# Performance work log

Hardware: AMD Instinct MI355X
Metric: run time of the kernel (lower is better)

Reference implementation:

```python
import jax, jax.numpy as jnp
import numpy as np
import math

H = 65
W = 65
NH = 8
DIM_K = 512
DIM_Q = 512
DIM_HID = NH * DIM_K  # 4096; forced by V.view(bsz,-1,num_heads,dim_K)
RW = W // 2 + 1  # 33, rfft2 last-dim size


def _conv2d(x, w, pad):
    # x: NCHW, w: OIHW
    return jax.lax.conv_general_dilated(
        x, w, window_strides=(1, 1), padding=[(pad, pad), (pad, pad)],
        dimension_numbers=('NCHW', 'OIHW', 'NCHW'))


def _filter_branch(x, w1, w2, w3, Wd, bd):
    # x: (1, DIM_K, H, W)
    f = _conv2d(x, w1, 0)                                  # 1x1 conv
    f = _conv2d(jax.nn.relu(f), w2, 1) + f                 # 3x3 conv + residual
    f = jax.nn.relu(_conv2d(jax.nn.relu(f), w3, 0))        # 1x1 -> (1, NH, H, W)
    f = f.reshape(NH, H * W) @ Wd.T + bd                   # down-proj to (NH, 65*33)
    return f.reshape(NH, H, RW)


def setup_inputs() -> dict:
    key = jax.random.key(0)
    ks = jax.random.split(key, 20)
    s = 0.02
    f32 = jnp.float32
    inp = {
        'Q': jax.random.normal(ks[0], (1, 1, DIM_Q), f32),
        'K': jax.random.normal(ks[1], (1, DIM_K, H, W), f32),
        'Wq': jax.random.normal(ks[2], (DIM_HID, DIM_Q), f32) * s,
        'bq': jnp.zeros((DIM_HID,), f32),
        'Wk': jax.random.normal(ks[3], (DIM_HID, DIM_K), f32) * s,
        'bk': jnp.zeros((DIM_HID,), f32),
        'Wv': jax.random.normal(ks[4], (DIM_HID, DIM_K), f32) * s,
        'bv': jnp.zeros((DIM_HID,), f32),
        'Wo': jax.random.normal(ks[5], (DIM_K, DIM_HID), f32) * s,
        'bo': jnp.zeros((DIM_K,), f32),
        'amp1': jax.random.normal(ks[6], (DIM_K, DIM_K, 1, 1), f32) * 0.05,
        'amp2': jax.random.normal(ks[7], (DIM_K, DIM_K, 3, 3), f32) * 0.02,
        'amp3': jax.random.normal(ks[8], (NH, DIM_K, 1, 1), f32) * 0.05,
        'pha1': jax.random.normal(ks[9], (DIM_K, DIM_K, 1, 1), f32) * 0.05,
        'pha2': jax.random.normal(ks[10], (DIM_K, DIM_K, 3, 3), f32) * 0.02,
        'pha3': jax.random.normal(ks[11], (NH, DIM_K, 1, 1), f32) * 0.05,
        'Wd1': jax.random.normal(ks[12], (H * RW, H * W), f32) * s,
        'bd1': jnp.zeros((H * RW,), f32),
        'Wd2': jax.random.normal(ks[13], (H * RW, H * W), f32) * s,
        'bd2': jnp.zeros((H * RW,), f32),
    }
    return inp


def reference(Q, K, Wq, bq, Wk, bk, Wv, bv, Wo, bo,
              amp1, amp2, amp3, pha1, pha2, pha3, Wd1, bd1, Wd2, bd2):
    bsz, h, w = K.shape[0], K.shape[2], K.shape[3]
    dk = DIM_HID // NH
    qrt = K
    Kp = jnp.transpose(K, (0, 2, 3, 1))                      # (1, h, w, DIM_K)
    q = Q @ Wq.T + bq                                        # (1, 1, DIM_HID)
    k = Kp @ Wk.T + bk                                       # (1, h, w, DIM_HID)
    v = Kp @ Wv.T + bv
    q = q.reshape(bsz, -1, NH, dk).transpose(0, 2, 1, 3)     # (1, NH, 1, dk)
    k = k.reshape(bsz, -1, NH, dk).transpose(0, 2, 1, 3)     # (1, NH, h*w, dk)
    v = v.reshape(bsz, -1, NH, DIM_K).transpose(0, 2, 1, 3)  # (1, NH, h*w, DIM_K)
    A = jnp.einsum('bhqd,bhkd->bhqk', q, k) / math.sqrt(DIM_K)
    amp_F = _filter_branch(qrt, amp1, amp2, amp3, Wd1, bd1)  # (NH, h, w//2+1)
    pha_F = _filter_branch(qrt, pha1, pha2, pha3, Wd2, bd2)
    A = A.reshape(NH, h, w)
    Af = jnp.fft.rfft2(A, axes=(-2, -1))                     # backward norm (default)
    amp = amp_F * jnp.abs(Af)
    pha = pha_F * jnp.angle(Af)
    Af = jax.lax.complex(amp * jnp.cos(pha), amp * jnp.sin(pha))
    A = jnp.fft.irfft2(Af, s=(h, w), axes=(-2, -1))
    A = jax.nn.softmax(A.reshape(bsz, NH, 1, -1), axis=-1)   # (1, NH, 1, h*w)
    x = jnp.einsum('bhqk,bhkd->bhqd', A, v)                  # (1, NH, 1, DIM_K)
    x = x.reshape(1, NH * DIM_K)
    return x @ Wo.T + bo                                     # (1, DIM_K)
```

## Files before the change

kernel.cpp:

```cpp
#include <hip/hip_runtime.h>
#include <hip/hip_bf16.h>

#define NP 4225
#define PR 2145

typedef __attribute__((ext_vector_type(8))) short short8;
typedef __attribute__((ext_vector_type(4))) float f32x4;
typedef __attribute__((ext_vector_type(4))) unsigned int u32x4;

__device__ inline float bf2f(unsigned short u) {
    union { unsigned int i; float f; } x; x.i = ((unsigned int)u) << 16; return x.f;
}
__device__ inline unsigned short f2bf(float f) {
    union { float f; unsigned int i; } x; x.f = f;
    unsigned int r = x.i + 0x7fff + ((x.i >> 16) & 1);
    return (unsigned short)(r >> 16);
}
__device__ inline u32x4 relu8(u32x4 v) {
    #pragma unroll
    for (int i = 0; i < 4; i++) {
        unsigned int s = v[i] & 0x80008000u;
        v[i] &= ~((s >> 15) * 0xFFFFu);
    }
    return v;
}


__global__ __launch_bounds__(256) void k_q(const float* __restrict__ Q,
                                           const float* __restrict__ Wq,
                                           const float* __restrict__ bq,
                                           float* __restrict__ qv)
{
    int wid = threadIdx.x >> 6, lane = threadIdx.x & 63;
    int j = blockIdx.x * 4 + wid;
    float s = 0.f;
    for (int i = lane; i < 512; i += 64) s += Q[i] * Wq[j * 512 + i];
    #pragma unroll
    for (int off = 32; off; off >>= 1) s += __shfl_down(s, off);
    if (lane == 0) qv[j] = s + bq[j];
}

__global__ __launch_bounds__(256) void k_qk3(const float* __restrict__ qv,
                                             const float* __restrict__ Wk,
                                             float* __restrict__ qkp)
{
    int c = blockIdx.x * 256 + threadIdx.x;
    int h = blockIdx.y, dz = blockIdx.z;
    __shared__ float qs[32];
    if (threadIdx.x < 32) qs[threadIdx.x] = qv[h * 512 + dz * 32 + threadIdx.x];
    __syncthreads();
    float s = 0.f;
    #pragma unroll 8
    for (int d = 0; d < 32; d++)
        s += qs[d] * Wk[(size_t)(h * 512 + dz * 32 + d) * 512 + c];
    qkp[(dz * 8 + h) * 512 + c] = s;
}

__global__ __launch_bounds__(512) void k_qb(const float* __restrict__ q,
                                            const float* __restrict__ bk,
                                            float* __restrict__ qb)
{
    int h = threadIdx.x >> 6, lane = threadIdx.x & 63;
    float s = 0.f;
    for (int d = lane; d < 512; d += 64) s += q[h * 512 + d] * bk[h * 512 + d];
    #pragma unroll
    for (int off = 32; off; off >>= 1) s += __shfl_down(s, off);
    if (lane == 0) qb[h] = s;
}

__global__ __launch_bounds__(256) void k_alogits3(const float* __restrict__ qkp,
                                                  const float* __restrict__ K,
                                                  float* __restrict__ Ap)
{
    __shared__ float sqk[8][16];
    int tid = threadIdx.x;
    int cz = blockIdx.y;
    if (tid < 128) {
        int hh = tid >> 4, cc = tid & 15;
        float s = 0.f;
        #pragma unroll
        for (int dz = 0; dz < 16; dz++) s += qkp[(dz * 8 + hh) * 512 + cz * 16 + cc];
        sqk[hh][cc] = s;
    }
    __syncthreads();
    int p = blockIdx.x * 256 + tid;
    bool ok = p < NP;
    float acc[8] = {};
    #pragma unroll
    for (int cc = 0; cc < 16; cc++) {
        float kv = ok ? K[(size_t)(cz * 16 + cc) * NP + p] : 0.f;
        #pragma unroll
        for (int h = 0; h < 8; h++) acc[h] += sqk[h][cc] * kv;
    }
    if (ok) {
        #pragma unroll
        for (int h = 0; h < 8; h++) Ap[(size_t)(cz * 8 + h) * NP + p] = acc[h];
    }
}

__global__ __launch_bounds__(256) void k_areduce(const float* __restrict__ Ap,
                                                 const float* __restrict__ qb,
                                                 float* __restrict__ A)
{
    int p = blockIdx.x * 256 + threadIdx.x;
    int h = blockIdx.y;
    if (p >= NP) return;
    float s = 0.f;
    #pragma unroll 8
    for (int cz = 0; cz < 32; cz++) s += Ap[(size_t)(cz * 8 + h) * NP + p];
    const float sc = 0.04419417382415922f;
    A[h * NP + p] = (s + qb[h]) * sc;
}


__global__ __launch_bounds__(256) void k_cast2(const float* __restrict__ a,
                                               const float* __restrict__ b,
                                               unsigned short* __restrict__ o)
{
    int i = blockIdx.x * 256 + threadIdx.x;
    int br = blockIdx.y;
    const float* src = br ? b : a;
    o[(size_t)br * 262144 + i] = f2bf(src[i]);
}

__global__ __launch_bounds__(256) void k_packW2(const float* __restrict__ a,
                                                const float* __restrict__ b,
                                                unsigned short* __restrict__ o)
{
    int i = blockIdx.x * 256 + threadIdx.x;
    int br = blockIdx.y;
    int m = i >> 9, c = i & 511;
    const float* src = (br ? b : a) + (size_t)i * 9;
    unsigned short* dst = o + (size_t)br * 512 * 4608;
    #pragma unroll
    for (int t = 0; t < 9; t++) dst[(size_t)m * 4608 + t * 512 + c] = f2bf(src[t]);
}


__global__ __launch_bounds__(256) void k_conv1T(const float* __restrict__ K,
                                                const unsigned short* __restrict__ w1b2,
                                                unsigned short* __restrict__ f0b2)
{
    __shared__ unsigned short As[2][64 * 64];
    __shared__ unsigned short Bs[2][128 * 64];
    int tid = threadIdx.x;
    int bid = blockIdx.x;
    int u = bid & 7;
    int t = bid >> 3;
    int bmi = u * 9 + t % 9;
    if (bmi >= 67) return;
    int combo = t / 9;
    int bm = bmi * 64;
    int bn = (combo & 3) * 128;
    int br = combo >> 2;
    const unsigned short* w1 = w1b2 + (size_t)br * 262144;
    unsigned short* f0 = f0b2 + (size_t)br * NP * 512;
    int lane = tid & 63;
    int w = tid >> 6;
    int wp = (w >> 1) * 32, wm = (w & 1) * 64;
    int rb = tid >> 1, hb = tid & 1;
    int ct = tid >> 4, p4 = (tid & 15) * 4;

    f32x4 acc[2][4];
    #pragma unroll
    for (int i = 0; i < 2; i++)
        #pragma unroll
        for (int j = 0; j < 4; j++) acc[i][j] = (f32x4){0.f, 0.f, 0.f, 0.f};

    float aA[16], aB[16];
    u32x4 bA[4], bB[4];

    auto loadRegs = [&](int kc, float (&ar)[16], u32x4 (&brg)[4]) {
        int c0 = kc * 64;
        #pragma unroll
        for (int pass = 0; pass < 4; pass++) {
            int cl = pass * 16 + ct;
            const float* src = K + (size_t)(c0 + cl) * NP + bm + p4;
            #pragma unroll
            for (int j = 0; j < 4; j++)
                ar[pass * 4 + j] = (bm + p4 + j < NP) ? src[j] : 0.f;
        }
        const unsigned short* brow = w1 + (size_t)(bn + rb) * 512 + c0 + hb * 32;
        #pragma unroll
        for (int j = 0; j < 4; j++) brg[j] = *(const u32x4*)(brow + j * 8);
    };
    auto writeS = [&](int buf, float (&ar)[16], u32x4 (&brg)[4]) {
        #pragma unroll
        for (int pass = 0; pass < 4; pass++) {
            int cl = pass * 16 + ct;
            #pragma unroll
            for (int j = 0; j < 4; j++) {
                int row = p4 + j;
                int byte = (row * 128 + cl * 2) ^ ((row & 7) << 4);
                *(unsigned short*)((char*)As[buf] + byte) = f2bf(ar[pass * 4 + j]);
            }
        }
        int bb = rb * 128 + hb * 64;
        #pragma unroll
        for (int j = 0; j < 4; j++)
            *(u32x4*)((char*)Bs[buf] + ((bb + j * 16) ^ ((rb & 7) << 4))) = brg[j];
    };
    auto mfmaStep = [&](int buf) {
        __builtin_amdgcn_s_setprio(1);
        #pragma unroll
        for (int ks = 0; ks < 2; ks++) {
            short8 af[2], bfr[4];
            #pragma unroll
            for (int fi = 0; fi < 2; fi++) {
                int row = wp + fi * 16 + (lane & 15);
                int byte = row * 128 + ((ks * 64 + ((lane >> 4) * 16)) ^ ((row & 7) << 4));
                af[fi] = *(const short8*)((char*)As[buf] + byte);
            }
            #pragma unroll
            for (int fj = 0; fj < 4; fj++) {
                int n = wm + fj * 16 + (lane & 15);
                int byte = n * 128 + ((ks * 64 + ((lane >> 4) * 16)) ^ ((n & 7) << 4));
                bfr[fj] = *(const short8*)((char*)Bs[buf] + byte);
            }
            #pragma unroll
            for (int fi = 0; fi < 2; fi++)
                #pragma unroll
                for (int fj = 0; fj < 4; fj++)
                    acc[fi][fj] = __builtin_amdgcn_mfma_f32_16x16x32_bf16(af[fi], bfr[fj], acc[fi][fj], 0, 0, 0);
        }
        __builtin_amdgcn_s_setprio(0);
    };

    loadRegs(0, aA, bA);
    loadRegs(1, aB, bB);
    writeS(0, aA, bA);
    __syncthreads();
    for (int ib = 0; ib < 4; ib++) {
        int it = 2 * ib;
        if (it + 2 < 8) loadRegs(it + 2, aA, bA);
        mfmaStep(0);
        writeS(1, aB, bB);
        __syncthreads();
        if (it + 3 < 8) loadRegs(it + 3, aB, bB);
        mfmaStep(1);
        if (it + 2 < 8) writeS(0, aA, bA);
        __syncthreads();
    }
    #pragma unroll
    for (int fi = 0; fi < 2; fi++)
        #pragma unroll
        for (int r = 0; r < 4; r++) {
            int p = bm + wp + fi * 16 + (lane >> 4) * 4 + r;
            if (p >= NP) continue;
            #pragma unroll
            for (int fj = 0; fj < 4; fj++) {
                int m = bn + wm + fj * 16 + (lane & 15);
                f0[(size_t)p * 512 + m] = f2bf(acc[fi][fj][r]);
            }
        }
}

__global__ __launch_bounds__(256) void k_conv3T(const unsigned short* __restrict__ f0b2,
                                                const unsigned short* __restrict__ w2b2,
                                                const float* __restrict__ amp3,
                                                const float* __restrict__ pha3,
                                                float* __restrict__ F2p)
{
    __shared__ unsigned short As[2][64 * 64];
    __shared__ unsigned short Bs[2][128 * 64];
    __shared__ float w3s[8 * 128];
    int tid = threadIdx.x;
    int bid = blockIdx.x;
    int u = bid & 7;
    int bmi = bid >> 3;
    if (bmi >= 67) return;
    int bm = bmi * 64;
    int bnq = u & 3;
    int bn = bnq * 128;
    int br = u >> 2;
    const unsigned short* f0 = f0b2 + (size_t)br * NP * 512;
    const unsigned short* w2 = w2b2 + (size_t)br * 512 * 4608;
    const float* w3 = br ? pha3 : amp3;
    for (int i = tid; i < 1024; i += 256) {
        int h = i >> 7, c = i & 127;
        w3s[i] = w3[h * 512 + bn + c];
    }
    int lane = tid & 63;
    int w = tid >> 6;
    int wp = (w >> 1) * 32, wm = (w & 1) * 64;
    int ra = tid >> 2, sa = tid & 3;
    int rb = tid >> 1, hb = tid & 1;
    int pA = bm + ra;
    int py = pA / 65, px = pA - py * 65;

    f32x4 acc[2][4];
    #pragma unroll
    for (int i = 0; i < 2; i++)
        #pragma unroll
        for (int j = 0; j < 4; j++) acc[i][j] = (f32x4){0.f, 0.f, 0.f, 0.f};

    u32x4 aA0, aA1, bA[4];
    u32x4 aB0, aB1, bB[4];

    auto loadRegs = [&](int it, u32x4& a0, u32x4& a1, u32x4 (&brg)[4]) {
        int kc = it / 9, tap = it - kc * 9;
        int ky = tap / 3 - 1, kx = tap % 3 - 1;
        int sy = py + ky, sx = px + kx;
        bool valid = (pA < NP) && sy >= 0 && sy < 65 && sx >= 0 && sx < 65;
        int srow = valid ? (pA + ky * 65 + kx) : 0;
        const unsigned short* arow = f0 + (size_t)srow * 512 + kc * 64 + sa * 16;
        u32x4 a0t = relu8(*(const u32x4*)arow);
        u32x4 a1t = relu8(*(const u32x4*)(arow + 8));
        a0 = valid ? a0t : (u32x4){0, 0, 0, 0};
        a1 = valid ? a1t : (u32x4){0, 0, 0, 0};
        const unsigned short* brow = w2 + tap * 512 + (size_t)(bn + rb) * 4608 + kc * 64 + hb * 32;
        #pragma unroll
        for (int j = 0; j < 4; j++) brg[j] = *(const u32x4*)(brow + j * 8);
    };
    auto writeS = [&](int buf, u32x4& a0, u32x4& a1, u32x4 (&brg)[4]) {
        int ab = ra * 128 + sa * 32;
        *(u32x4*)((char*)As[buf] + ((ab) ^ ((ra & 7) << 4)))      = a0;
        *(u32x4*)((char*)As[buf] + ((ab + 16) ^ ((ra & 7) << 4))) = a1;
        int bb = rb * 128 + hb * 64;
        #pragma unroll
        for (int j = 0; j < 4; j++)
            *(u32x4*)((char*)Bs[buf] + ((bb + j * 16) ^ ((rb & 7) << 4))) = brg[j];
    };
    auto mfmaStep = [&](int buf) {
        __builtin_amdgcn_s_setprio(1);
        #pragma unroll
        for (int ks = 0; ks < 2; ks++) {
            short8 af[2], bfr[4];
            #pragma unroll
            for (int fi = 0; fi < 2; fi++) {
                int row = wp + fi * 16 + (lane & 15);
                int byte = row * 128 + ((ks * 64 + ((lane >> 4) * 16)) ^ ((row & 7) << 4));
                af[fi] = *(const short8*)((char*)As[buf] + byte);
            }
            #pragma unroll
            for (int fj = 0; fj < 4; fj++) {
                int n = wm + fj * 16 + (lane & 15);
                int byte = n * 128 + ((ks * 64 + ((lane >> 4) * 16)) ^ ((n & 7) << 4));
                bfr[fj] = *(const short8*)((char*)Bs[buf] + byte);
            }
            #pragma unroll
            for (int fi = 0; fi < 2; fi++)
                #pragma unroll
                for (int fj = 0; fj < 4; fj++)
                    acc[fi][fj] = __builtin_amdgcn_mfma_f32_16x16x32_bf16(af[fi], bfr[fj], acc[fi][fj], 0, 0, 0);
        }
        __builtin_amdgcn_s_setprio(0);
    };

    loadRegs(0, aA0, aA1, bA);
    loadRegs(1, aB0, aB1, bB);
    writeS(0, aA0, aA1, bA);
    __syncthreads();
    for (int ib = 0; ib < 36; ib++) {
        int it = 2 * ib;
        if (it + 2 < 72) loadRegs(it + 2, aA0, aA1, bA);
        mfmaStep(0);
        writeS(1, aB0, aB1, bB);
        __syncthreads();
        if (it + 3 < 72) loadRegs(it + 3, aB0, aB1, bB);
        mfmaStep(1);
        if (it + 2 < 72) writeS(0, aA0, aA1, bA);
        __syncthreads();
    }
    #pragma unroll
    for (int fi = 0; fi < 2; fi++)
        #pragma unroll
        for (int r = 0; r < 4; r++) {
            int row = wp + fi * 16 + (lane >> 4) * 4 + r;
            int p = bm + row;
            #pragma unroll
            for (int fj = 0; fj < 4; fj++) {
                int mcol = wm + fj * 16 + (lane & 15);
                float v = 0.f;
                if (p < NP)
                    v = fmaxf(acc[fi][fj][r] + bf2f(f0[(size_t)p * 512 + bn + mcol]), 0.f);
                int byte = (row * 256 + mcol * 2) ^ ((row & 7) << 4);
                *(unsigned short*)((char*)Bs[0] + byte) = f2bf(v);
            }
        }
    __syncthreads();
    int pl = tid >> 2, qc = tid & 3;
    float a8[8] = {};
    #pragma unroll 4
    for (int jj = 0; jj < 16; jj++) {
        int c = qc * 32 + jj * 2;
        int byte = (pl * 256 + c * 2) ^ ((pl & 7) << 4);
        unsigned int uu = *(const unsigned int*)((char*)Bs[0] + byte);
        float v0 = bf2f((unsigned short)(uu & 0xFFFF));
        float v1 = bf2f((unsigned short)(uu >> 16));
        #pragma unroll
        for (int h = 0; h < 8; h++)
            a8[h] += w3s[h * 128 + c] * v0 + w3s[h * 128 + c + 1] * v1;
    }
    #pragma unroll
    for (int h = 0; h < 8; h++) {
        a8[h] += __shfl_xor(a8[h], 1);
        a8[h] += __shfl_xor(a8[h], 2);
    }
    int p = bm + pl;
    if (qc == 0 && p < NP) {
        float* dst = F2p + (size_t)(br * 4 + bnq) * 8 * NP;
        #pragma unroll
        for (int h = 0; h < 8; h++) dst[h * NP + p] = a8[h];
    }
}

__global__ __launch_bounds__(256) void k_f2red(const float* __restrict__ F2p,
                                               float* __restrict__ F2)
{
    int p = blockIdx.x * 256 + threadIdx.x;
    int h = blockIdx.y, br = blockIdx.z;
    if (p >= NP) return;
    float s = 0.f;
    #pragma unroll
    for (int bn = 0; bn < 4; bn++) s += F2p[(size_t)((br * 4 + bn) * 8 + h) * NP + p];
    F2[(size_t)(br * 8 + h) * NP + p] = fmaxf(s, 0.f);
}

__global__ __launch_bounds__(256) void k_down(const float* __restrict__ F2,
                                              const float* __restrict__ Wd1,
                                              const float* __restrict__ bd1,
                                              const float* __restrict__ Wd2,
                                              const float* __restrict__ bd2,
                                              float* __restrict__ Fa,
                                              float* __restrict__ Fp)
{
    int wid = threadIdx.x >> 6, lane = threadIdx.x & 63;
    int j = blockIdx.x * 4 + wid;
    if (j >= PR) return;
    int br = blockIdx.y;
    const float* Wd = br ? Wd2 : Wd1;
    const float* bd = br ? bd2 : bd1;
    const float* F2b = F2 + (size_t)br * 8 * NP;
    float* Fo = br ? Fp : Fa;
    const float* wr = Wd + (size_t)j * NP;
    float acc[8] = {};
    for (int p = lane; p < NP; p += 64) {
        float wv = wr[p];
        #pragma unroll
        for (int h = 0; h < 8; h++) acc[h] += wv * F2b[h * NP + p];
    }
    #pragma unroll
    for (int h = 0; h < 8; h++) {
        #pragma unroll
        for (int off = 32; off; off >>= 1) acc[h] += __shfl_down(acc[h], off);
    }
    if (lane == 0) {
        float b = bd[j];
        #pragma unroll
        for (int h = 0; h < 8; h++) Fo[h * PR + j] = acc[h] + b;
    }
}


__global__ __launch_bounds__(128) void k_twid(double* __restrict__ ctd, double* __restrict__ snd,
                                              float* __restrict__ ctf, float* __restrict__ stf)
{
    int t = threadIdx.x;
    if (t < 65) {
        double ang = 6.283185307179586476925286766559 * (double)t / 65.0;
        double cv = cos(ang), sv = sin(ang);
        ctd[t] = cv; snd[t] = sv;
        ctf[t] = (float)cv; stf[t] = (float)sv;
    }
}

__global__ __launch_bounds__(64) void k_fftA(const float* __restrict__ A,
                                             const double* __restrict__ ctd,
                                             const double* __restrict__ snd,
                                             float* __restrict__ TrG, float* __restrict__ TiG)
{
    int b = blockIdx.x;
    int h = b / 65, y = b % 65;
    int lane = threadIdx.x;
    __shared__ float rowA[65];
    __shared__ double c65[65], s65[65];
    rowA[lane] = A[h * NP + y * 65 + lane];
    c65[lane] = ctd[lane]; s65[lane] = snd[lane];
    if (lane == 0) {
        rowA[64] = A[h * NP + y * 65 + 64];
        c65[64] = ctd[64]; s65[64] = snd[64];
    }
    __syncthreads();
    int v = lane;
    if (v < 33) {
        double sr = 0.0, si = 0.0;
        for (int x = 0; x < 65; x++) {
            int m = (v * x) % 65;
            double a = (double)rowA[x];
            sr += a * c65[m];
            si -= a * s65[m];
        }
        TrG[(h * 65 + y) * 33 + v] = (float)sr;
        TiG[(h * 65 + y) * 33 + v] = (float)si;
    }
}

__global__ __launch_bounds__(128) void k_fftBC(const float* __restrict__ TrG,
                                               const float* __restrict__ TiG,
                                               const float* __restrict__ Fa,
                                               const float* __restrict__ Fp,
                                               const double* __restrict__ ctd,
                                               const double* __restrict__ snd,
                                               const float* __restrict__ ctf,
                                               const float* __restrict__ stf,
                                               float* __restrict__ CrG, float* __restrict__ CiG)
{
    int v = blockIdx.x, h = blockIdx.y;
    int t = threadIdx.x;
    __shared__ float TrS[65], TiS[65];
    __shared__ float BrS[65], BiS[65];
    __shared__ double c65[65], s65[65];
    __shared__ float cf[65], sf[65];
    if (t < 65) {
        TrS[t] = TrG[(h * 65 + t) * 33 + v];
        TiS[t] = TiG[(h * 65 + t) * 33 + v];
        c65[t] = ctd[t]; s65[t] = snd[t];
        cf[t] = ctf[t]; sf[t] = stf[t];
    }
    __syncthreads();
    int uu = t;
    if (uu < 65) {
        double sr = 0.0, si = 0.0;
        for (int y = 0; y < 65; y++) {
            int m = (uu * y) % 65;
            double c = c65[m], s = s65[m];
            double tr = (double)TrS[y], ti = (double)TiS[y];
            sr += tr * c + ti * s;
            si += ti * c - tr * s;
        }
        float re = (float)sr, im = (float)si;
        float mag = sqrtf(re * re + im * im);
        float ang = atan2f(im, re);
        int o = uu * 33 + v;
        float amp = Fa[h * PR + o] * mag;
        float ph  = Fp[h * PR + o] * ang;
        float sn, cn;
        sincosf(ph, &sn, &cn);
        BrS[uu] = amp * cn;
        BiS[uu] = amp * sn;
    }
    __syncthreads();
    int y = t;
    if (y < 65) {
        float sr = 0.f, si = 0.f;
        for (int u2 = 0; u2 < 65; u2++) {
            int m = (u2 * y) % 65;
            float c = cf[m], s = sf[m];
            float ar = BrS[u2], ai = BiS[u2];
            sr += ar * c - ai * s;
            si += ai * c + ar * s;
        }
        CrG[(h * 65 + y) * 33 + v] = sr;
        CiG[(h * 65 + y) * 33 + v] = si;
    }
}

__global__ __launch_bounds__(128) void k_fftD(const float* __restrict__ CrG,
                                              const float* __restrict__ CiG,
                                              const float* __restrict__ ctf,
                                              const float* __restrict__ stf,
                                              float* __restrict__ A2)
{
    int y = blockIdx.x, h = blockIdx.y;
    int t = threadIdx.x;
    __shared__ float CrS[33], CiS[33];
    __shared__ float c65[65], s65[65];
    if (t < 33) {
        CrS[t] = CrG[(h * 65 + y) * 33 + t];
        CiS[t] = CiG[(h * 65 + y) * 33 + t];
    }
    if (t < 65) { c65[t] = ctf[t]; s65[t] = stf[t]; }
    __syncthreads();
    int x = t;
    if (x < 65) {
        float s = CrS[0];
        for (int v = 1; v < 33; v++) {
            int m = (v * x) % 65;
            s += 2.f * (CrS[v] * c65[m] - CiS[v] * s65[m]);
        }
        A2[h * NP + y * 65 + x] = s * (1.f / 4225.f);
    }
}

__global__ __launch_bounds__(1024) void k_softmax(const float* __restrict__ A2,
                                                  float* __restrict__ Wsm)
{
    int h = blockIdx.x, tid = threadIdx.x;
    __shared__ float red[1024];
    float mx = -3.0e38f;
    for (int i = tid; i < NP; i += 1024) mx = fmaxf(mx, A2[h * NP + i]);
    red[tid] = mx; __syncthreads();
    for (int s = 512; s; s >>= 1) {
        if (tid < s) red[tid] = fmaxf(red[tid], red[tid + s]);
        __syncthreads();
    }
    mx = red[0]; __syncthreads();
    float sum = 0.f;
    for (int i = tid; i < NP; i += 1024) sum += expf(A2[h * NP + i] - mx);
    red[tid] = sum; __syncthreads();
    for (int s = 512; s; s >>= 1) {
        if (tid < s) red[tid] += red[tid + s];
        __syncthreads();
    }
    float inv = 1.f / red[0];
    for (int i = tid; i < NP; i += 1024) Wsm[h * NP + i] = expf(A2[h * NP + i] - mx) * inv;
}

__global__ __launch_bounds__(256) void k_t(const float* __restrict__ K,
                                           const float* __restrict__ Wsm,
                                           float* __restrict__ t)
{
    int wid = threadIdx.x >> 6, lane = threadIdx.x & 63;
    int c = blockIdx.x * 4 + wid;
    float acc[8] = {};
    for (int p = lane; p < NP; p += 64) {
        float kv = K[(size_t)c * NP + p];
        #pragma unroll
        for (int h = 0; h < 8; h++) acc[h] += kv * Wsm[h * NP + p];
    }
    #pragma unroll
    for (int h = 0; h < 8; h++) {
        #pragma unroll
        for (int off = 32; off; off >>= 1) acc[h] += __shfl_down(acc[h], off);
    }
    if (lane == 0) {
        #pragma unroll
        for (int h = 0; h < 8; h++) t[h * 512 + c] = acc[h];
    }
}

__global__ __launch_bounds__(256) void k_x(const float* __restrict__ t,
                                           const float* __restrict__ Wv,
                                           const float* __restrict__ bv,
                                           float* __restrict__ x)
{
    int wid = threadIdx.x >> 6, lane = threadIdx.x & 63;
    int hd = blockIdx.x * 4 + wid;
    int h = hd >> 9;
    float s = 0.f;
    for (int c = lane; c < 512; c += 64) s += t[h * 512 + c] * Wv[(size_t)hd * 512 + c];
    #pragma unroll
    for (int off = 32; off; off >>= 1) s += __shfl_down(s, off);
    if (lane == 0) x[hd] = s + bv[hd];
}

__global__ __launch_bounds__(256) void k_out(const float* __restrict__ x,
                                             const float* __restrict__ Wo,
                                             const float* __restrict__ bo,
                                             float* __restrict__ out)
{
    int wid = threadIdx.x >> 6, lane = threadIdx.x & 63;
    int j = blockIdx.x * 4 + wid;
    float s = 0.f;
    for (int i = lane; i < 4096; i += 64) s += x[i] * Wo[(size_t)j * 4096 + i];
    #pragma unroll
    for (int off = 32; off; off >>= 1) s += __shfl_down(s, off);
    if (lane == 0) out[j] = s + bo[j];
}

extern "C" void kernel_launch(void* const* d_in, const int* in_sizes, int n_in,
                              void* d_out, int out_size, void* d_ws, size_t ws_size,
                              hipStream_t stream)
{
    (void)in_sizes; (void)n_in; (void)out_size; (void)ws_size;
    const float* Q    = (const float*)d_in[0];
    const float* K    = (const float*)d_in[1];
    const float* Wq   = (const float*)d_in[2];
    const float* bq   = (const float*)d_in[3];
    const float* Wk   = (const float*)d_in[4];
    const float* bk   = (const float*)d_in[5];
    const float* Wv   = (const float*)d_in[6];
    const float* bv   = (const float*)d_in[7];
    const float* Wo   = (const float*)d_in[8];
    const float* bo   = (const float*)d_in[9];
    const float* amp1 = (const float*)d_in[10];
    const float* amp2 = (const float*)d_in[11];
    const float* amp3 = (const float*)d_in[12];
    const float* pha1 = (const float*)d_in[13];
    const float* pha2 = (const float*)d_in[14];
    const float* pha3 = (const float*)d_in[15];
    const float* Wd1  = (const float*)d_in[16];
    const float* bd1  = (const float*)d_in[17];
    const float* Wd2  = (const float*)d_in[18];
    const float* bd2  = (const float*)d_in[19];
    float* out = (float*)d_out;

    char* w = (char*)d_ws;
    auto alloc = [&](size_t bytes) { char* p = w; w += (bytes + 255) & ~(size_t)255; return p; };
    float* qv   = (float*)alloc(4096 * 4);
    float* qkp  = (float*)alloc(16 * 8 * 512 * 4);
    float* qb   = (float*)alloc(64 * 4);
    float* A    = (float*)alloc(8 * NP * 4);
    unsigned short* w1b2 = (unsigned short*)alloc((size_t)2 * 512 * 512 * 2);
    unsigned short* w2b2 = (unsigned short*)alloc((size_t)2 * 512 * 4608 * 2);
    unsigned short* f0b2 = (unsigned short*)alloc((size_t)2 * NP * 512 * 2);
    float* F2p  = (float*)alloc((size_t)2 * 4 * 8 * NP * 4);
    float* F2   = (float*)alloc((size_t)2 * 8 * NP * 4);
    float* Fa   = (float*)alloc(8 * PR * 4);
    float* Fp   = (float*)alloc(8 * PR * 4);
    double* ctd = (double*)alloc(65 * 8);
    double* snd = (double*)alloc(65 * 8);
    float* ctf  = (float*)alloc(65 * 4);
    float* stf  = (float*)alloc(65 * 4);
    float* Ap   = (float*)w2b2;
    {
        char* s2 = (char*)f0b2;
        auto alias = [&](size_t bytes) { char* p = s2; s2 += (bytes + 255) & ~(size_t)255; return p; };
        float* A2  = (float*)alias(8 * NP * 4);
        float* wsm = (float*)alias(8 * NP * 4);
        float* tt  = (float*)alias(4096 * 4);
        float* xx  = (float*)alias(4096 * 4);
        float* TrG = (float*)alias(8 * PR * 4);
        float* TiG = (float*)alias(8 * PR * 4);
        float* CrG = (float*)alias(8 * PR * 4);
        float* CiG = (float*)alias(8 * PR * 4);

        k_twid<<<1, 128, 0, stream>>>(ctd, snd, ctf, stf);

        k_q<<<1024, 256, 0, stream>>>(Q, Wq, bq, qv);
        k_qk3<<<dim3(2, 8, 16), 256, 0, stream>>>(qv, Wk, qkp);
        k_qb<<<1, 512, 0, stream>>>(qv, bk, qb);
        k_alogits3<<<dim3(17, 32), 256, 0, stream>>>(qkp, K, Ap);
        k_areduce<<<dim3(17, 8), 256, 0, stream>>>(Ap, qb, A);

        k_cast2<<<dim3(1024, 2), 256, 0, stream>>>(amp1, pha1, w1b2);
        k_packW2<<<dim3(1024, 2), 256, 0, stream>>>(amp2, pha2, w2b2);

        k_conv1T<<<576, 256, 0, stream>>>(K, w1b2, f0b2);
        k_conv3T<<<576, 256, 0, stream>>>(f0b2, w2b2, amp3, pha3, F2p);
        k_f2red<<<dim3(17, 8, 2), 256, 0, stream>>>(F2p, F2);
        k_down<<<dim3(537, 2), 256, 0, stream>>>(F2, Wd1, bd1, Wd2, bd2, Fa, Fp);

        k_fftA<<<520, 64, 0, stream>>>(A, ctd, snd, TrG, TiG);
        k_fftBC<<<dim3(33, 8), 128, 0, stream>>>(TrG, TiG, Fa, Fp, ctd, snd, ctf, stf, CrG, CiG);
        k_fftD<<<dim3(65, 8), 128, 0, stream>>>(CrG, CiG, ctf, stf, A2);
        k_softmax<<<8, 1024, 0, stream>>>(A2, wsm);
        k_t<<<128, 256, 0, stream>>>(K, wsm, tt);
        k_x<<<1024, 256, 0, stream>>>(tt, Wv, bv, xx);
        k_out<<<128, 256, 0, stream>>>(xx, Wo, bo, out);
    }
}
```

Before: 259.4 us.

## Stage halo input tile in LDS once per channel chunk for 3x3 conv

```diff
diff --git a/kernel.cpp b/kernel.cpp
--- a/kernel.cpp
+++ b/kernel.cpp
@@ -261,7 +261,7 @@
                                                 const float* __restrict__ pha3,
                                                 float* __restrict__ F2p)
 {
-    __shared__ unsigned short As[2][64 * 64];
+    __shared__ unsigned short Ah[196 * 64];
     __shared__ unsigned short Bs[2][128 * 64];
     __shared__ float w3s[8 * 128];
     int tid = threadIdx.x;
@@ -283,10 +283,9 @@
     int lane = tid & 63;
     int w = tid >> 6;
     int wp = (w >> 1) * 32, wm = (w & 1) * 64;
-    int ra = tid >> 2, sa = tid & 3;
     int rb = tid >> 1, hb = tid & 1;
-    int pA = bm + ra;
-    int py = pA / 65, px = pA - py * 65;
+    int pxf0 = (bm + wp + (lane & 15)) % 65;
+    int pxf1 = (bm + wp + 16 + (lane & 15)) % 65;
 
     f32x4 acc[2][4];
     #pragma unroll
@@ -294,44 +293,54 @@
         #pragma unroll
         for (int j = 0; j < 4; j++) acc[i][j] = (f32x4){0.f, 0.f, 0.f, 0.f};
 
-    u32x4 aA0, aA1, bA[4];
-    u32x4 aB0, aB1, bB[4];
-
-    auto loadRegs = [&](int it, u32x4& a0, u32x4& a1, u32x4 (&brg)[4]) {
-        int kc = it / 9, tap = it - kc * 9;
-        int ky = tap / 3 - 1, kx = tap % 3 - 1;
-        int sy = py + ky, sx = px + kx;
-        bool valid = (pA < NP) && sy >= 0 && sy < 65 && sx >= 0 && sx < 65;
-        int srow = valid ? (pA + ky * 65 + kx) : 0;
-        const unsigned short* arow = f0 + (size_t)srow * 512 + kc * 64 + sa * 16;
-        u32x4 a0t = relu8(*(const u32x4*)arow);
-        u32x4 a1t = relu8(*(const u32x4*)(arow + 8));
-        a0 = valid ? a0t : (u32x4){0, 0, 0, 0};
-        a1 = valid ? a1t : (u32x4){0, 0, 0, 0};
+    u32x4 rB0[4], rB1[4];
+
+    auto stageAh = [&](int kc) {
+        for (int i = tid; i < 196 * 4; i += 256) {
+            int row = i >> 2, seg = i & 3;
+            int g = bm - 66 + row;
+            u32x4 v0 = {0, 0, 0, 0}, v1 = {0, 0, 0, 0};
+            if (g >= 0 && g < NP) {
+                const unsigned short* src = f0 + (size_t)g * 512 + kc * 64 + seg * 16;
+                v0 = relu8(*(const u32x4*)src);
+                v1 = relu8(*(const u32x4*)(src + 8));
+            }
+            int byte = row * 128 + seg * 32;
+            int swz = (row & 7) << 4;
+            *(u32x4*)((char*)Ah + (byte ^ swz)) = v0;
+            *(u32x4*)((char*)Ah + ((byte + 16) ^ swz)) = v1;
+        }
+    };
+    auto loadB = [&](int s, u32x4 (&brg)[4]) {
+        int kc = s / 9, tap = s - kc * 9;
         const unsigned short* brow = w2 + tap * 512 + (size_t)(bn + rb) * 4608 + kc * 64 + hb * 32;
         #pragma unroll
         for (int j = 0; j < 4; j++) brg[j] = *(const u32x4*)(brow + j * 8);
     };
-    auto writeS = [&](int buf, u32x4& a0, u32x4& a1, u32x4 (&brg)[4]) {
-        int ab = ra * 128 + sa * 32;
-        *(u32x4*)((char*)As[buf] + ((ab) ^ ((ra & 7) << 4)))      = a0;
-        *(u32x4*)((char*)As[buf] + ((ab + 16) ^ ((ra & 7) << 4))) = a1;
+    auto writeB = [&](int buf, u32x4 (&brg)[4]) {
         int bb = rb * 128 + hb * 64;
         #pragma unroll
         for (int j = 0; j < 4; j++)
             *(u32x4*)((char*)Bs[buf] + ((bb + j * 16) ^ ((rb & 7) << 4))) = brg[j];
     };
-    auto mfmaStep = [&](int buf) {
+    auto mfmaTap = [&](int buf, int tap) {
+        int ky = tap / 3 - 1, kx = tap % 3 - 1;
+        int dR = 66 + ky * 65 + kx;
+        short8 zero8 = {0, 0, 0, 0, 0, 0, 0, 0};
+        bool cut0 = (kx < 0 && pxf0 == 0) || (kx > 0 && pxf0 == 64);
+        bool cut1 = (kx < 0 && pxf1 == 0) || (kx > 0 && pxf1 == 64);
         __builtin_amdgcn_s_setprio(1);
         #pragma unroll
         for (int ks = 0; ks < 2; ks++) {
             short8 af[2], bfr[4];
             #pragma unroll
             for (int fi = 0; fi < 2; fi++) {
-                int row = wp + fi * 16 + (lane & 15);
-                int byte = row * 128 + ((ks * 64 + ((lane >> 4) * 16)) ^ ((row & 7) << 4));
-                af[fi] = *(const short8*)((char*)As[buf] + byte);
+                int hrow = wp + fi * 16 + (lane & 15) + dR;
+                int byte = hrow * 128 + ((ks * 64 + ((lane >> 4) * 16)) ^ ((hrow & 7) << 4));
+                af[fi] = *(const short8*)((char*)Ah + byte);
             }
+            if (cut0) af[0] = zero8;
+            if (cut1) af[1] = zero8;
             #pragma unroll
             for (int fj = 0; fj < 4; fj++) {
                 int n = wm + fj * 16 + (lane & 15);
@@ -347,19 +356,23 @@
         __builtin_amdgcn_s_setprio(0);
     };
 
-    loadRegs(0, aA0, aA1, bA);
-    loadRegs(1, aB0, aB1, bB);
-    writeS(0, aA0, aA1, bA);
+    loadB(0, rB0);
+    loadB(1, rB1);
+    stageAh(0);
+    writeB(0, rB0);
     __syncthreads();
     for (int ib = 0; ib < 36; ib++) {
-        int it = 2 * ib;
-        if (it + 2 < 72) loadRegs(it + 2, aA0, aA1, bA);
-        mfmaStep(0);
-        writeS(1, aB0, aB1, bB);
+        int s0 = 2 * ib;
+        if (s0 > 0 && s0 % 9 == 0) { stageAh(s0 / 9); __syncthreads(); }
+        if (s0 + 2 < 72) loadB(s0 + 2, rB0);
+        mfmaTap(0, s0 % 9);
+        writeB(1, rB1);
         __syncthreads();
-        if (it + 3 < 72) loadRegs(it + 3, aB0, aB1, bB);
-        mfmaStep(1);
-        if (it + 2 < 72) writeS(0, aA0, aA1, bA);
+        int s1 = s0 + 1;
+        if (s1 % 9 == 0) { stageAh(s1 / 9); __syncthreads(); }
+        if (s1 + 2 < 72) loadB(s1 + 2, rB1);
+        mfmaTap(1, s1 % 9);
+        if (s1 + 1 < 72) writeB(0, rB0);
         __syncthreads();
     }
     #pragma unroll
```

Result: slower. 291.4 us (+12.3%).

## Stage conv weight tiles via direct global-to-LDS loads with pre-swizzled packing

Applied to the files above, without the earlier changes.

```diff
diff --git a/kernel.cpp b/kernel.cpp
--- a/kernel.cpp
+++ b/kernel.cpp
@@ -23,6 +23,12 @@
         v[i] &= ~((s >> 15) * 0xFFFFu);
     }
     return v;
+}
+__device__ inline void gl_lds16(const void* g, void* l) {
+    __builtin_amdgcn_global_load_lds(
+        (const __attribute__((address_space(1))) unsigned int*)g,
+        (__attribute__((address_space(3))) unsigned int*)l,
+        16, 0, 0);
 }
 
 
@@ -120,7 +126,9 @@
     int i = blockIdx.x * 256 + threadIdx.x;
     int br = blockIdx.y;
     const float* src = br ? b : a;
-    o[(size_t)br * 262144 + i] = f2bf(src[i]);
+    int m = i >> 9, c = i & 511;
+    int dst = (c & ~63) | ((c & 63) ^ ((m & 7) << 3));
+    o[(size_t)br * 262144 + m * 512 + dst] = f2bf(src[i]);
 }
 
 __global__ __launch_bounds__(256) void k_packW2(const float* __restrict__ a,
@@ -132,8 +140,9 @@
     int m = i >> 9, c = i & 511;
     const float* src = (br ? b : a) + (size_t)i * 9;
     unsigned short* dst = o + (size_t)br * 512 * 4608;
-    #pragma unroll
-    for (int t = 0; t < 9; t++) dst[(size_t)m * 4608 + t * 512 + c] = f2bf(src[t]);
+    int cs = (c & ~63) | ((c & 63) ^ ((m & 7) << 3));
+    #pragma unroll
+    for (int t = 0; t < 9; t++) dst[(size_t)m * 4608 + t * 512 + cs] = f2bf(src[t]);
 }
 
 
@@ -158,33 +167,35 @@
     int lane = tid & 63;
     int w = tid >> 6;
     int wp = (w >> 1) * 32, wm = (w & 1) * 64;
-    int rb = tid >> 1, hb = tid & 1;
     int ct = tid >> 4, p4 = (tid & 15) * 4;
 
+    bool okj[4];
+    int colj[4];
+    #pragma unroll
+    for (int j = 0; j < 4; j++) {
+        okj[j] = (bm + p4 + j) < NP;
+        colj[j] = okj[j] ? (p4 + j) : (NP - 1 - bm);
+    }
+
     f32x4 acc[2][4];
     #pragma unroll
     for (int i = 0; i < 2; i++)
         #pragma unroll
         for (int j = 0; j < 4; j++) acc[i][j] = (f32x4){0.f, 0.f, 0.f, 0.f};
 
-    float aA[16], aB[16];
-    u32x4 bA[4], bB[4];
-
-    auto loadRegs = [&](int kc, float (&ar)[16], u32x4 (&brg)[4]) {
+    float aE[16], aO[16];
+
+    auto loadA = [&](int kc, float (&ar)[16]) {
         int c0 = kc * 64;
         #pragma unroll
         for (int pass = 0; pass < 4; pass++) {
             int cl = pass * 16 + ct;
-            const float* src = K + (size_t)(c0 + cl) * NP + bm + p4;
-            #pragma unroll
-            for (int j = 0; j < 4; j++)
-                ar[pass * 4 + j] = (bm + p4 + j < NP) ? src[j] : 0.f;
-        }
-        const unsigned short* brow = w1 + (size_t)(bn + rb) * 512 + c0 + hb * 32;
-        #pragma unroll
-        for (int j = 0; j < 4; j++) brg[j] = *(const u32x4*)(brow + j * 8);
+            const float* src = K + (size_t)(c0 + cl) * NP + bm;
+            #pragma unroll
+            for (int j = 0; j < 4; j++) ar[pass * 4 + j] = src[colj[j]];
+        }
     };
-    auto writeS = [&](int buf, float (&ar)[16], u32x4 (&brg)[4]) {
+    auto writeA = [&](int buf, float (&ar)[16]) {
         #pragma unroll
         for (int pass = 0; pass < 4; pass++) {
             int cl = pass * 16 + ct;
@@ -192,13 +203,19 @@
             for (int j = 0; j < 4; j++) {
                 int row = p4 + j;
                 int byte = (row * 128 + cl * 2) ^ ((row & 7) << 4);
-                *(unsigned short*)((char*)As[buf] + byte) = f2bf(ar[pass * 4 + j]);
+                float v = okj[j] ? ar[pass * 4 + j] : 0.f;
+                *(unsigned short*)((char*)As[buf] + byte) = f2bf(v);
             }
         }
-        int bb = rb * 128 + hb * 64;
-        #pragma unroll
-        for (int j = 0; j < 4; j++)
-            *(u32x4*)((char*)Bs[buf] + ((bb + j * 16) ^ ((rb & 7) << 4))) = brg[j];
+    };
+    auto stageB = [&](int kc, int buf) {
+        const unsigned short* gb = w1 + (size_t)kc * 64 + (lane & 7) * 8;
+        #pragma unroll
+        for (int j = 0; j < 4; j++) {
+            int row = (w * 4 + j) * 8 + (lane >> 3);
+            gl_lds16(gb + (size_t)(bn + row) * 512,
+                     (char*)Bs[buf] + (w * 4 + j) * 1024);
+        }
     };
     auto mfmaStep = [&](int buf) {
         __builtin_amdgcn_s_setprio(1);
@@ -226,19 +243,24 @@
         __builtin_amdgcn_s_setprio(0);
     };
 
-    loadRegs(0, aA, bA);
-    loadRegs(1, aB, bB);
-    writeS(0, aA, bA);
-    __syncthreads();
+    loadA(0, aE);
+    loadA(1, aO);
+    stageB(0, 0);
+    writeA(0, aE);
+    __syncthreads();
+    #pragma unroll
     for (int ib = 0; ib < 4; ib++) {
-        int it = 2 * ib;
-        if (it + 2 < 8) loadRegs(it + 2, aA, bA);
+        int s0 = 2 * ib;
+        if (s0 + 1 < 8) stageB(s0 + 1, 1);
+        if (s0 + 2 < 8) loadA(s0 + 2, aE);
         mfmaStep(0);
-        writeS(1, aB, bB);
+        if (s0 + 1 < 8) writeA(1, aO);
         __syncthreads();
-        if (it + 3 < 8) loadRegs(it + 3, aB, bB);
+        int s1 = s0 + 1;
+        if (s1 + 1 < 8) stageB(s1 + 1, 0);
+        if (s1 + 2 < 8) loadA(s1 + 2, aO);
         mfmaStep(1);
-        if (it + 2 < 8) writeS(0, aA, bA);
+        if (s1 + 1 < 8) writeA(0, aE);
         __syncthreads();
     }
     #pragma unroll
@@ -284,7 +306,6 @@
     int w = tid >> 6;
     int wp = (w >> 1) * 32, wm = (w & 1) * 64;
     int ra = tid >> 2, sa = tid & 3;
-    int rb = tid >> 1, hb = tid & 1;
     int pA = bm + ra;
     int py = pA / 65, px = pA - py * 65;
 
@@ -294,32 +315,38 @@
         #pragma unroll
         for (int j = 0; j < 4; j++) acc[i][j] = (f32x4){0.f, 0.f, 0.f, 0.f};
 
-    u32x4 aA0, aA1, bA[4];
-    u32x4 aB0, aB1, bB[4];
-
-    auto loadRegs = [&](int it, u32x4& a0, u32x4& a1, u32x4 (&brg)[4]) {
-        int kc = it / 9, tap = it - kc * 9;
+    u32x4 aE0, aE1, aO0, aO1;
+    bool vE, vO;
+
+    auto loadA = [&](int s, u32x4& a0, u32x4& a1, bool& vv) {
+        int kc = s / 9, tap = s - kc * 9;
         int ky = tap / 3 - 1, kx = tap % 3 - 1;
         int sy = py + ky, sx = px + kx;
         bool valid = (pA < NP) && sy >= 0 && sy < 65 && sx >= 0 && sx < 65;
         int srow = valid ? (pA + ky * 65 + kx) : 0;
         const unsigned short* arow = f0 + (size_t)srow * 512 + kc * 64 + sa * 16;
-        u32x4 a0t = relu8(*(const u32x4*)arow);
-        u32x4 a1t = relu8(*(const u32x4*)(arow + 8));
-        a0 = valid ? a0t : (u32x4){0, 0, 0, 0};
-        a1 = valid ? a1t : (u32x4){0, 0, 0, 0};
-        const unsigned short* brow = w2 + tap * 512 + (size_t)(bn + rb) * 4608 + kc * 64 + hb * 32;
-        #pragma unroll
-        for (int j = 0; j < 4; j++) brg[j] = *(const u32x4*)(brow + j * 8);
+        a0 = *(const u32x4*)arow;
+        a1 = *(const u32x4*)(arow + 8);
+        vv = valid;
     };
-    auto writeS = [&](int buf, u32x4& a0, u32x4& a1, u32x4 (&brg)[4]) {
+    auto writeA = [&](int buf, u32x4 a0, u32x4 a1, bool vv) {
+        u32x4 z = {0, 0, 0, 0};
+        u32x4 w0 = vv ? relu8(a0) : z;
+        u32x4 w1 = vv ? relu8(a1) : z;
         int ab = ra * 128 + sa * 32;
-        *(u32x4*)((char*)As[buf] + ((ab) ^ ((ra & 7) << 4)))      = a0;
-        *(u32x4*)((char*)As[buf] + ((ab + 16) ^ ((ra & 7) << 4))) = a1;
-        int bb = rb * 128 + hb * 64;
-        #pragma unroll
-        for (int j = 0; j < 4; j++)
-            *(u32x4*)((char*)Bs[buf] + ((bb + j * 16) ^ ((rb & 7) << 4))) = brg[j];
+        int swz = (ra & 7) << 4;
+        *(u32x4*)((char*)As[buf] + (ab ^ swz)) = w0;
+        *(u32x4*)((char*)As[buf] + ((ab + 16) ^ swz)) = w1;
+    };
+    auto stageB = [&](int s, int buf) {
+        int kc = s / 9, tap = s - kc * 9;
+        const unsigned short* gb = w2 + (size_t)tap * 512 + kc * 64 + (lane & 7) * 8;
+        #pragma unroll
+        for (int j = 0; j < 4; j++) {
+            int row = (w * 4 + j) * 8 + (lane >> 3);
+            gl_lds16(gb + (size_t)(bn + row) * 4608,
+                     (char*)Bs[buf] + (w * 4 + j) * 1024);
+        }
     };
     auto mfmaStep = [&](int buf) {
         __builtin_amdgcn_s_setprio(1);
@@ -347,19 +374,23 @@
         __builtin_amdgcn_s_setprio(0);
     };
 
-    loadRegs(0, aA0, aA1, bA);
-    loadRegs(1, aB0, aB1, bB);
-    writeS(0, aA0, aA1, bA);
+    loadA(0, aE0, aE1, vE);
+    loadA(1, aO0, aO1, vO);
+    stageB(0, 0);
+    writeA(0, aE0, aE1, vE);
     __syncthreads();
     for (int ib = 0; ib < 36; ib++) {
-        int it = 2 * ib;
-        if (it + 2 < 72) loadRegs(it + 2, aA0, aA1, bA);
+        int s0 = 2 * ib;
+        if (s0 + 1 < 72) stageB(s0 + 1, 1);
+        if (s0 + 2 < 72) loadA(s0 + 2, aE0, aE1, vE);
         mfmaStep(0);
-        writeS(1, aB0, aB1, bB);
+        if (s0 + 1 < 72) writeA(1, aO0, aO1, vO);
         __syncthreads();
-        if (it + 3 < 72) loadRegs(it + 3, aB0, aB1, bB);
+        int s1 = s0 + 1;
+        if (s1 + 1 < 72) stageB(s1 + 1, 0);
+        if (s1 + 2 < 72) loadA(s1 + 2, aO0, aO1, vO);
         mfmaStep(1);
-        if (it + 2 < 72) writeS(0, aA0, aA1, bA);
+        if (s1 + 1 < 72) writeA(0, aE0, aE1, vE);
         __syncthreads();
     }
     #pragma unroll
@@ -728,7 +759,7 @@
         k_packW2<<<dim3(1024, 2), 256, 0, stream>>>(amp2, pha2, w2b2);
 
         k_conv1T<<<576, 256, 0, stream>>>(K, w1b2, f0b2);
-        k_conv3T<<<576, 256, 0, stream>>>(f0b2, w2b2, amp3, pha3, F2p);
+        k_conv3T<<<536, 256, 0, stream>>>(f0b2, w2b2, amp3, pha3, F2p);
         k_f2red<<<dim3(17, 8, 2), 256, 0, stream>>>(F2p, F2);
         k_down<<<dim3(537, 2), 256, 0, stream>>>(F2, Wd1, bd1, Wd2, bd2, Fa, Fp);
 
```

After: 252.4 us. 1.03x faster.
